# Optimization experiments

Measured on AMD Instinct MI355X. Metric: run time of the kernel, lower is better.

## Reference

```python
import jax, jax.numpy as jnp
import numpy as np

H = 512   # embedding_dim (forced by Attention(512,512))
F = 21    # n_features
T = 28    # output_length

def _cell(x, h, c, Wih, Whh, b):
    # PyTorch LSTMCell math, gate order i,f,g,o
    g = x @ Wih.T + h @ Whh.T + b
    i, f, gg, o = jnp.split(g, 4, axis=-1)
    c2 = jax.nn.sigmoid(f) * c + jax.nn.sigmoid(i) * jnp.tanh(gg)
    h2 = jax.nn.sigmoid(o) * jnp.tanh(c2)
    return h2, c2

def _lstm3(inp, h, c, Wih0, Wih1, Wih2, Whh, bih, bhh):
    # 3-layer LSTM, single time step. h,c: [3,1,H]
    Wihs = (Wih0, Wih1, Wih2)
    hs, cs = [], []
    x = inp
    for l in range(3):
        hl, cl = _cell(x, h[l], c[l], Wihs[l], Whh[l], bih[l] + bhh[l])
        hs.append(hl); cs.append(cl)
        x = hl
    return x, jnp.stack(hs), jnp.stack(cs)

def setup_inputs() -> dict:
    key = jax.random.key(0)
    ks = jax.random.split(key, 20)
    s = 0.05
    f32 = jnp.float32
    return {
        "x": jax.random.normal(ks[0], (1, F), f32),
        "prev_y": jax.random.normal(ks[1], (1, F), f32),
        "enc_Wih0": jax.random.normal(ks[2], (4*H, F), f32) * s,
        "enc_Wih1": jax.random.normal(ks[3], (4*H, H), f32) * s,
        "enc_Wih2": jax.random.normal(ks[4], (4*H, H), f32) * s,
        "enc_Whh": jax.random.normal(ks[5], (3, 4*H, H), f32) * s,
        "enc_bih": jax.random.normal(ks[6], (3, 4*H), f32) * s,
        "enc_bhh": jax.random.normal(ks[7], (3, 4*H), f32) * s,
        "attn_W": jax.random.normal(ks[8], (H, 2*H), f32) * s,
        "attn_b": jax.random.normal(ks[9], (H,), f32) * s,
        "v_W": jax.random.normal(ks[10], (1, H), f32) * s,
        "dec_Wih0": jax.random.normal(ks[11], (4*H, H+F), f32) * s,
        "dec_Wih1": jax.random.normal(ks[12], (4*H, H), f32) * s,
        "dec_Wih2": jax.random.normal(ks[13], (4*H, H), f32) * s,
        "dec_Whh": jax.random.normal(ks[14], (3, 4*H, H), f32) * s,
        "dec_bih": jax.random.normal(ks[15], (3, 4*H), f32) * s,
        "dec_bhh": jax.random.normal(ks[16], (3, 4*H), f32) * s,
        "out_W": jax.random.normal(ks[17], (F, 2*H), f32) * s,
        "out_b": jax.random.normal(ks[18], (F,), f32) * s,
    }

def reference(x, prev_y, enc_Wih0, enc_Wih1, enc_Wih2, enc_Whh, enc_bih, enc_bhh,
              attn_W, attn_b, v_W, dec_Wih0, dec_Wih1, dec_Wih2, dec_Whh, dec_bih, dec_bhh,
              out_W, out_b):
    z = jnp.zeros((3, 1, H), x.dtype)
    # Encoder: single time step over feature-as-sequence input [1, F]
    enc_out, h, c = _lstm3(x, z, z, enc_Wih0, enc_Wih1, enc_Wih2, enc_Whh, enc_bih, enc_bhh)
    # enc_out: [1, H]; src_len == 1

    def step(carry, _):
        prev_out, h, c = carry
        # Bahdanau attention (src_len = 1)
        cat = jnp.concatenate([h[2], enc_out], axis=-1)          # [1, 2H]
        energy = jnp.tanh(cat @ attn_W.T + attn_b)               # [1, H]
        score = energy @ v_W.T                                    # [1, 1]
        a = jax.nn.softmax(score, axis=1)                         # [1, 1] (== 1)
        weighted = a * enc_out                                    # [1, H]
        rnn_in = jnp.concatenate([prev_out, weighted], axis=-1)  # [1, H+F]
        out, h2, c2 = _lstm3(rnn_in, h, c, dec_Wih0, dec_Wih1, dec_Wih2, dec_Whh, dec_bih, dec_bhh)
        y = jnp.concatenate([out, weighted], axis=-1) @ out_W.T + out_b  # [1, F]
        return (y, h2, c2), y

    _, ys = jax.lax.scan(step, (prev_y, h, c), None, length=T)
    return ys  # [T, 1, F]
```

## Files before the change

kernel.cpp:

```cpp
#include <hip/hip_runtime.h>
#include <cstddef>

constexpr int H  = 512;
constexpr int F  = 21;
constexpr int T  = 28;
constexpr int PB = 128;
constexpr int NB = PB + 1;
constexpr int NT = 256;
constexpr int NW = NT / 64;

#define SCOPE_AGENT __HIP_MEMORY_SCOPE_AGENT

__device__ unsigned long long g_hp[2][3][H];
__device__ unsigned long long g_hy[T][H];
__device__ unsigned g_exit;

struct P {
  const float *x, *py, *eW0, *eW1, *eW2, *ebih, *ebhh;
  const float *dW0, *dW1, *dW2, *dWhh, *dbih, *dbhh, *outW, *outb;
  float* out;
};

__device__ __forceinline__ float sigm(float v)  { return 1.0f / (1.0f + __expf(-v)); }
__device__ __forceinline__ float tanh_f(float v){ return 1.0f - 2.0f / (__expf(2.0f * v) + 1.0f); }

__device__ __forceinline__ float4 wredsum4(float4 v) {
#pragma unroll
  for (int off = 32; off > 0; off >>= 1) {
    v.x += __shfl_xor(v.x, off, 64);
    v.y += __shfl_xor(v.y, off, 64);
    v.z += __shfl_xor(v.z, off, 64);
    v.w += __shfl_xor(v.w, off, 64);
  }
  return v;
}
__device__ __forceinline__ float wredsum1(float v) {
#pragma unroll
  for (int off = 32; off > 0; off >>= 1) v += __shfl_xor(v, off, 64);
  return v;
}

__device__ __forceinline__ void pput(unsigned long long* slot, float v, unsigned tag) {
  union { float f; unsigned u; } c; c.f = v;
  unsigned long long pk = ((unsigned long long)tag << 32) | (unsigned long long)c.u;
  (void)__hip_atomic_exchange(slot, pk, __ATOMIC_RELAXED, SCOPE_AGENT);
}
__device__ __forceinline__ unsigned long long tld(const unsigned long long* q) {
  return __hip_atomic_load(q, __ATOMIC_RELAXED, SCOPE_AGENT);
}
__device__ __forceinline__ float fbits(unsigned long long v) {
  union { unsigned u; float f; } c; c.u = (unsigned)v; return c.f;
}

__device__ __forceinline__ void stagev(const unsigned long long* __restrict__ A,
                                       unsigned wa, float* __restrict__ dst) {
  const int i = threadIdx.x;
  unsigned long long v0 = tld(A + i), v1 = tld(A + i + NT);
  int guard = 0;
  while ((((unsigned)(v0 >> 32)) != wa || ((unsigned)(v1 >> 32)) != wa) &&
         ++guard < (1 << 20)) {
    v0 = tld(A + i); v1 = tld(A + i + NT);
  }
  dst[i] = fbits(v0); dst[i + NT] = fbits(v1);
  __syncthreads();
}

struct W8 { float4 a[4]; float4 b[4]; };

__device__ __forceinline__ W8 ldw_g(const float* __restrict__ W, int r, int lane) {
  W8 o;
#pragma unroll
  for (int g = 0; g < 4; ++g) {
    const float* q = W + (size_t)(g * H + r) * H + lane * 8;
    o.a[g] = *(const float4*)q;
    o.b[g] = *(const float4*)(q + 4);
  }
  return o;
}
__device__ __forceinline__ W8 ldw_lds(const float* sM, int w, int lane) {
  W8 o;
#pragma unroll
  for (int g = 0; g < 4; ++g) {
    const float* q = sM + (w * 4 + g) * H + lane * 8;
    o.a[g] = *(const float4*)q;
    o.b[g] = *(const float4*)(q + 4);
  }
  return o;
}
__device__ __forceinline__ void fma8(const W8& wt, const float4& x0, const float4& x1,
                                     float s[4]) {
#pragma unroll
  for (int g = 0; g < 4; ++g) {
    s[g] += wt.a[g].x * x0.x + wt.a[g].y * x0.y + wt.a[g].z * x0.z + wt.a[g].w * x0.w
          + wt.b[g].x * x1.x + wt.b[g].y * x1.y + wt.b[g].z * x1.z + wt.b[g].w * x1.w;
  }
}

__device__ __forceinline__ float cellup(const float4& v, const float b[4], float& c) {
  float cn = sigm(v.y + b[1]) * c + sigm(v.x + b[0]) * tanh_f(v.z + b[2]);
  c = cn;
  return sigm(v.w + b[3]) * tanh_f(cn);
}

__device__ __forceinline__ void write_y_frag(const P& p, int trow, int w, int lane,
                                             const float4& h0, const float4& h1,
                                             const float* sYe) {
  for (int j = w; j < F; j += NW) {
    const float* q = p.outW + (size_t)j * (2 * H) + lane * 8;
    float4 w0 = *(const float4*)q;
    float4 w1 = *(const float4*)(q + 4);
    float s = w0.x * h0.x + w0.y * h0.y + w0.z * h0.z + w0.w * h0.w
            + w1.x * h1.x + w1.y * h1.y + w1.z * h1.z + w1.w * h1.w;
    s = wredsum1(s);
    if (lane == 0) p.out[trow * F + j] = s + sYe[j];
  }
}

__global__ __launch_bounds__(NT, 1)
void k_flow(P p) {
  const int lane = threadIdx.x & 63;
  const int w    = threadIdx.x >> 6;

  __shared__ float sM[NW * 4 * H];
  __shared__ float sBuf[2][H];
  __shared__ float senc[H];
  __shared__ float sYe[F + 3];
  __shared__ int   s_last;

  if (blockIdx.x == PB) {
    stagev(g_hp[1][2], 1u, senc);
    {
      float4 e0 = *(const float4*)(senc + lane * 8);
      float4 e1 = *(const float4*)(senc + lane * 8 + 4);
      for (int j = w; j < F; j += NW) {
        const float* q = p.outW + (size_t)j * (2 * H) + H + lane * 8;
        float4 w0 = *(const float4*)q;
        float4 w1 = *(const float4*)(q + 4);
        float s = w0.x * e0.x + w0.y * e0.y + w0.z * e0.z + w0.w * e0.w
                + w1.x * e1.x + w1.y * e1.y + w1.z * e1.z + w1.w * e1.w;
        s = wredsum1(s);
        if (lane == 0) sYe[j] = s + p.outb[j];
      }
      __syncthreads();
    }
    for (int t = 0; t < T; ++t) {
      float* xb = sBuf[t & 1];
      stagev(g_hy[t], (unsigned)(t + 2), xb);
      float4 h20 = *(const float4*)(xb + lane * 8);
      float4 h21 = *(const float4*)(xb + lane * 8 + 4);
      write_y_frag(p, t, w, lane, h20, h21, sYe);
    }
  } else {
    const int r = blockIdx.x * NW + w;

    float c0 = 0.f, c1 = 0.f, c2 = 0.f;
    float b00[4], b0p[4], b1s[4], b2s[4];
    float sOld0[4] = {0, 0, 0, 0}, sOld1[4] = {0, 0, 0, 0}, sOld2[4] = {0, 0, 0, 0};
    int bi = 0;

    {
      float s0 = 0.f, s1 = 0.f, s2 = 0.f, s3 = 0.f;
      if (lane < F) {
        const float xv = p.x[lane];
        s0 = p.eW0[(size_t)(0 * H + r) * F + lane] * xv;
        s1 = p.eW0[(size_t)(1 * H + r) * F + lane] * xv;
        s2 = p.eW0[(size_t)(2 * H + r) * F + lane] * xv;
        s3 = p.eW0[(size_t)(3 * H + r) * F + lane] * xv;
      }
      float4 v = wredsum4(make_float4(s0, s1, s2, s3));
      if (lane == 0) {
        const float* bi_ = p.ebih + r;
        const float* bh_ = p.ebhh + r;
        float cn = sigm(v.x + bi_[0] + bh_[0]) * tanh_f(v.z + bi_[2 * H] + bh_[2 * H]);
        c0 = cn;
        pput(&g_hp[1][0][r], sigm(v.w + bi_[3 * H] + bh_[3 * H]) * tanh_f(cn), 1u);
      }
    }

    {
      float4 mA[4], mB[4];
#pragma unroll
      for (int g = 0; g < 4; ++g) {
        mA[g] = make_float4(0.f, 0.f, 0.f, 0.f);
        mB[g] = make_float4(0.f, 0.f, 0.f, 0.f);
      }
      for (int f = 0; f < F; ++f) {
        const float* q = p.outW + (size_t)f * (2 * H) + lane * 8;
        const float4 oa = *(const float4*)q;
        const float4 ob = *(const float4*)(q + 4);
#pragma unroll
        for (int g = 0; g < 4; ++g) {
          const float wf = p.dW0[(size_t)(g * H + r) * (H + F) + f];
          mA[g].x += wf * oa.x; mA[g].y += wf * oa.y; mA[g].z += wf * oa.z; mA[g].w += wf * oa.w;
          mB[g].x += wf * ob.x; mB[g].y += wf * ob.y; mB[g].z += wf * ob.z; mB[g].w += wf * ob.w;
        }
      }
#pragma unroll
      for (int g = 0; g < 4; ++g) {
        *(float4*)(sM + (w * 4 + g) * H + lane * 8)     = mA[g];
        *(float4*)(sM + (w * 4 + g) * H + lane * 8 + 4) = mB[g];
      }
    }
#pragma unroll
    for (int g = 0; g < 4; ++g) {
      b1s[g] = p.dbih[4 * H + g * H + r] + p.dbhh[4 * H + g * H + r];
      b2s[g] = p.dbih[8 * H + g * H + r] + p.dbhh[8 * H + g * H + r];
    }

    {
      W8 wt = ldw_g(p.eW1, r, lane);
      stagev(g_hp[1][0], 1u, sBuf[0]);
      float4 a0 = *(const float4*)(sBuf[0] + lane * 8);
      float4 a1 = *(const float4*)(sBuf[0] + lane * 8 + 4);
      float s[4] = {0.f, 0.f, 0.f, 0.f};
      fma8(wt, a0, a1, s);
      float4 v = wredsum4(make_float4(s[0], s[1], s[2], s[3]));
      if (lane == 0) {
        const float* bi_ = p.ebih + 4 * H + r;
        const float* bh_ = p.ebhh + 4 * H + r;
        float cn = sigm(v.x + bi_[0] + bh_[0]) * tanh_f(v.z + bi_[2 * H] + bh_[2 * H]);
        c1 = cn;
        pput(&g_hp[1][1][r], sigm(v.w + bi_[3 * H] + bh_[3 * H]) * tanh_f(cn), 1u);
      }
    }

    {
      W8 wt  = ldw_g(p.eW2, r, lane);
      W8 wh1 = ldw_g(p.dWhh + (size_t)4 * H * H, r, lane);
      stagev(g_hp[1][1], 1u, sBuf[1]);
      float4 a0 = *(const float4*)(sBuf[1] + lane * 8);
      float4 a1 = *(const float4*)(sBuf[1] + lane * 8 + 4);
      float s[4] = {0.f, 0.f, 0.f, 0.f};
      fma8(wt, a0, a1, s);
      float4 v = wredsum4(make_float4(s[0], s[1], s[2], s[3]));
      if (lane == 0) {
        const float* bi_ = p.ebih + 8 * H + r;
        const float* bh_ = p.ebhh + 8 * H + r;
        float cn = sigm(v.x + bi_[0] + bh_[0]) * tanh_f(v.z + bi_[2 * H] + bh_[2 * H]);
        c2 = cn;
        pput(&g_hp[1][2][r], sigm(v.w + bi_[3 * H] + bh_[3 * H]) * tanh_f(cn), 1u);
      }
      fma8(wh1, a0, a1, sOld1);
    }

    {
      W8 wh2 = ldw_g(p.dWhh + (size_t)8 * H * H, r, lane);
      stagev(g_hp[1][2], 1u, senc);
      float4 e0 = *(const float4*)(senc + lane * 8);
      float4 e1 = *(const float4*)(senc + lane * 8 + 4);
      for (int j = w; j < F; j += NW) {
        const float* q = p.outW + (size_t)j * (2 * H) + H + lane * 8;
        float4 w0 = *(const float4*)q;
        float4 w1 = *(const float4*)(q + 4);
        float s = w0.x * e0.x + w0.y * e0.y + w0.z * e0.z + w0.w * e0.w
                + w1.x * e1.x + w1.y * e1.y + w1.z * e1.z + w1.w * e1.w;
        s = wredsum1(s);
        if (lane == 0) sYe[j] = s + p.outb[j];
      }
      {
        float sg[4];
#pragma unroll
        for (int g = 0; g < 4; ++g) {
          const float* q = p.dW0 + (size_t)(g * H + r) * (H + F) + F + lane * 8;
          sg[g] = q[0] * e0.x + q[1] * e0.y + q[2] * e0.z + q[3] * e0.w
                + q[4] * e1.x + q[5] * e1.y + q[6] * e1.z + q[7] * e1.w;
        }
        float4 v = wredsum4(make_float4(sg[0], sg[1], sg[2], sg[3]));
        if (lane == 0) {
          b0p[0] = v.x + p.dbih[0 * H + r] + p.dbhh[0 * H + r];
          b0p[1] = v.y + p.dbih[1 * H + r] + p.dbhh[1 * H + r];
          b0p[2] = v.z + p.dbih[2 * H + r] + p.dbhh[2 * H + r];
          b0p[3] = v.w + p.dbih[3 * H + r] + p.dbhh[3 * H + r];
        }
      }
      {
        float f0 = 0.f, f1 = 0.f, f2 = 0.f, f3 = 0.f;
        if (lane < F) {
          const float yv = p.py[lane];
          f0 = p.dW0[(size_t)(0 * H + r) * (H + F) + lane] * yv;
          f1 = p.dW0[(size_t)(1 * H + r) * (H + F) + lane] * yv;
          f2 = p.dW0[(size_t)(2 * H + r) * (H + F) + lane] * yv;
          f3 = p.dW0[(size_t)(3 * H + r) * (H + F) + lane] * yv;
        }
        float4 v = wredsum4(make_float4(f0, f1, f2, f3));
        if (lane == 0) {
          b00[0] = b0p[0] + v.x; b00[1] = b0p[1] + v.y;
          b00[2] = b0p[2] + v.z; b00[3] = b0p[3] + v.w;
        }
      }
      __syncthreads();
      {
        float f0 = 0.f, f1 = 0.f, f2 = 0.f, f3 = 0.f;
        if (lane < F) {
          const float yv = sYe[lane];
          f0 = p.dW0[(size_t)(0 * H + r) * (H + F) + lane] * yv;
          f1 = p.dW0[(size_t)(1 * H + r) * (H + F) + lane] * yv;
          f2 = p.dW0[(size_t)(2 * H + r) * (H + F) + lane] * yv;
          f3 = p.dW0[(size_t)(3 * H + r) * (H + F) + lane] * yv;
        }
        float4 v = wredsum4(make_float4(f0, f1, f2, f3));
        if (lane == 0) {
          b0p[0] += v.x; b0p[1] += v.y; b0p[2] += v.z; b0p[3] += v.w;
        }
      }
      fma8(wh2, e0, e1, sOld2);
    }

    {
      W8 wh0 = ldw_g(p.dWhh, r, lane);
      float4 a0 = *(const float4*)(sBuf[0] + lane * 8);
      float4 a1 = *(const float4*)(sBuf[0] + lane * 8 + 4);
      float s[4] = {0.f, 0.f, 0.f, 0.f};
      fma8(wh0, a0, a1, s);
      float4 v = wredsum4(make_float4(s[0], s[1], s[2], s[3]));
      if (lane == 0) pput(&g_hp[0][0][r], cellup(v, b00, c0), 2u);
    }
    __syncthreads();

    for (int t = 0; t < T; ++t) {
      const int pb = t & 1, ob = pb ^ 1;
      const unsigned wn = (unsigned)(t + 2);
      const unsigned wo = (unsigned)(t + 1);

      if (t >= 1) {
        W8 wh2 = ldw_g(p.dWhh + (size_t)8 * H * H, r, lane);
        stagev(g_hp[ob][2], wo, sBuf[bi]);
        W8 wm = ldw_lds(sM, w, lane);
        float4 h20 = *(const float4*)(sBuf[bi] + lane * 8);
        float4 h21 = *(const float4*)(sBuf[bi] + lane * 8 + 4);
        float s[4] = {sOld0[0], sOld0[1], sOld0[2], sOld0[3]};
        fma8(wm, h20, h21, s);
        float4 v = wredsum4(make_float4(s[0], s[1], s[2], s[3]));
        if (lane == 0) pput(&g_hp[pb][0][r], cellup(v, b0p, c0), wn);
        sOld2[0] = sOld2[1] = sOld2[2] = sOld2[3] = 0.f;
        fma8(wh2, h20, h21, sOld2);
        bi ^= 1;
      }

      {
        W8 wi  = ldw_g(p.dW1, r, lane);
        W8 wh0 = ldw_g(p.dWhh, r, lane);
        stagev(g_hp[pb][0], wn, sBuf[bi]);
        float4 a0 = *(const float4*)(sBuf[bi] + lane * 8);
        float4 a1 = *(const float4*)(sBuf[bi] + lane * 8 + 4);
        float s[4] = {sOld1[0], sOld1[1], sOld1[2], sOld1[3]};
        fma8(wi, a0, a1, s);
        float4 v = wredsum4(make_float4(s[0], s[1], s[2], s[3]));
        if (lane == 0) pput(&g_hp[pb][1][r], cellup(v, b1s, c1), wn);
        sOld0[0] = sOld0[1] = sOld0[2] = sOld0[3] = 0.f;
        fma8(wh0, a0, a1, sOld0);
        bi ^= 1;
      }
      {
        W8 wi  = ldw_g(p.dW2, r, lane);
        W8 wh1 = ldw_g(p.dWhh + (size_t)4 * H * H, r, lane);
        stagev(g_hp[pb][1], wn, sBuf[bi]);
        float4 a0 = *(const float4*)(sBuf[bi] + lane * 8);
        float4 a1 = *(const float4*)(sBuf[bi] + lane * 8 + 4);
        float s[4] = {sOld2[0], sOld2[1], sOld2[2], sOld2[3]};
        fma8(wi, a0, a1, s);
        float4 v = wredsum4(make_float4(s[0], s[1], s[2], s[3]));
        if (lane == 0) {
          float hv = cellup(v, b2s, c2);
          pput(&g_hp[pb][2][r], hv, wn);
          pput(&g_hy[t][r], hv, wn);
        }
        sOld1[0] = sOld1[1] = sOld1[2] = sOld1[3] = 0.f;
        fma8(wh1, a0, a1, sOld1);
        bi ^= 1;
      }
    }
  }

  __syncthreads();
  if (threadIdx.x == 0) {
    unsigned old = __hip_atomic_fetch_add(&g_exit, 1u, __ATOMIC_RELAXED, SCOPE_AGENT);
    s_last = (old == NB - 1) ? 1 : 0;
  }
  __syncthreads();
  if (s_last) {
    unsigned long long* z = &g_hp[0][0][0];
    for (int i = threadIdx.x; i < 2 * 3 * H; i += NT)
      __hip_atomic_store(z + i, 0ull, __ATOMIC_RELAXED, SCOPE_AGENT);
    unsigned long long* y = &g_hy[0][0];
    for (int i = threadIdx.x; i < T * H; i += NT)
      __hip_atomic_store(y + i, 0ull, __ATOMIC_RELAXED, SCOPE_AGENT);
    if (threadIdx.x == 0)
      __hip_atomic_store(&g_exit, 0u, __ATOMIC_RELAXED, SCOPE_AGENT);
  }
}

extern "C" void kernel_launch(void* const* d_in, const int* in_sizes, int n_in,
                              void* d_out, int out_size, void* d_ws, size_t ws_size,
                              hipStream_t stream) {
  P p;
  p.x    = (const float*)d_in[0];
  p.py   = (const float*)d_in[1];
  p.eW0  = (const float*)d_in[2];
  p.eW1  = (const float*)d_in[3];
  p.eW2  = (const float*)d_in[4];
  p.ebih = (const float*)d_in[6];
  p.ebhh = (const float*)d_in[7];
  p.dW0  = (const float*)d_in[11];
  p.dW1  = (const float*)d_in[12];
  p.dW2  = (const float*)d_in[13];
  p.dWhh = (const float*)d_in[14];
  p.dbih = (const float*)d_in[15];
  p.dbhh = (const float*)d_in[16];
  p.outW = (const float*)d_in[17];
  p.outb = (const float*)d_in[18];
  p.out  = (float*)d_out;

  hipLaunchKernelGGL(k_flow, dim3(NB), dim3(NT), 0, stream, p);
}
```

Measured before the change: 319.6 us.

## Epoch-tag flags, vectorize polling loads, keep weights in registers, drop exit cleanup

The per-launch zeroing of the flag arrays at kernel exit is replaced by an epoch counter folded into the tags, which removes the end-of-kernel atomic count and reset pass. Flag polling now uses a single 16-byte load with the sc1 cache bit per thread instead of two 8-byte atomic loads. The fused output-to-input matrix and the W1/W2 tiles stay in registers across all steps instead of being reread from LDS and global memory. Stage waits are moved ahead of the remaining weight loads. This raises register pressure and relies on the epoch never wrapping into stale tags.

```diff
diff --git a/kernel.cpp b/kernel.cpp
--- a/kernel.cpp
+++ b/kernel.cpp
@@ -11,9 +11,9 @@
 
 #define SCOPE_AGENT __HIP_MEMORY_SCOPE_AGENT
 
-__device__ unsigned long long g_hp[2][3][H];
-__device__ unsigned long long g_hy[T][H];
-__device__ unsigned g_exit;
+__device__ __align__(16) unsigned long long g_hp[2][3][H];
+__device__ __align__(16) unsigned long long g_hy[T][H];
+__device__ unsigned g_epoch;
 
 struct P {
   const float *x, *py, *eW0, *eW1, *eW2, *ebih, *ebhh;
@@ -45,23 +45,23 @@
   unsigned long long pk = ((unsigned long long)tag << 32) | (unsigned long long)c.u;
   (void)__hip_atomic_exchange(slot, pk, __ATOMIC_RELAXED, SCOPE_AGENT);
 }
-__device__ __forceinline__ unsigned long long tld(const unsigned long long* q) {
-  return __hip_atomic_load(q, __ATOMIC_RELAXED, SCOPE_AGENT);
-}
-__device__ __forceinline__ float fbits(unsigned long long v) {
-  union { unsigned u; float f; } c; c.u = (unsigned)v; return c.f;
+
+typedef unsigned int u32x4 __attribute__((ext_vector_type(4)));
+__device__ __forceinline__ u32x4 tld16(const unsigned long long* q) {
+  u32x4 r;
+  asm volatile("global_load_dwordx4 %0, %1, off sc1\n\t"
+               "s_waitcnt vmcnt(0)"
+               : "=v"(r) : "v"(q) : "memory");
+  return r;
 }
 
 __device__ __forceinline__ void stagev(const unsigned long long* __restrict__ A,
                                        unsigned wa, float* __restrict__ dst) {
   const int i = threadIdx.x;
-  unsigned long long v0 = tld(A + i), v1 = tld(A + i + NT);
+  u32x4 v = tld16(A + 2 * i);
   int guard = 0;
-  while ((((unsigned)(v0 >> 32)) != wa || ((unsigned)(v1 >> 32)) != wa) &&
-         ++guard < (1 << 20)) {
-    v0 = tld(A + i); v1 = tld(A + i + NT);
-  }
-  dst[i] = fbits(v0); dst[i + NT] = fbits(v1);
+  while ((v.y != wa || v.w != wa) && ++guard < (1 << 20)) v = tld16(A + 2 * i);
+  *(float2*)(dst + 2 * i) = make_float2(__uint_as_float(v.x), __uint_as_float(v.z));
   __syncthreads();
 }
 
@@ -72,16 +72,6 @@
 #pragma unroll
   for (int g = 0; g < 4; ++g) {
     const float* q = W + (size_t)(g * H + r) * H + lane * 8;
-    o.a[g] = *(const float4*)q;
-    o.b[g] = *(const float4*)(q + 4);
-  }
-  return o;
-}
-__device__ __forceinline__ W8 ldw_lds(const float* sM, int w, int lane) {
-  W8 o;
-#pragma unroll
-  for (int g = 0; g < 4; ++g) {
-    const float* q = sM + (w * 4 + g) * H + lane * 8;
     o.a[g] = *(const float4*)q;
     o.b[g] = *(const float4*)(q + 4);
   }
@@ -120,15 +110,15 @@
 void k_flow(P p) {
   const int lane = threadIdx.x & 63;
   const int w    = threadIdx.x >> 6;
-
-  __shared__ float sM[NW * 4 * H];
+  const unsigned ep =
+      __hip_atomic_load(&g_epoch, __ATOMIC_RELAXED, SCOPE_AGENT) << 6;
+
   __shared__ float sBuf[2][H];
   __shared__ float senc[H];
   __shared__ float sYe[F + 3];
-  __shared__ int   s_last;
 
   if (blockIdx.x == PB) {
-    stagev(g_hp[1][2], 1u, senc);
+    stagev(g_hp[1][2], ep + 1u, senc);
     {
       float4 e0 = *(const float4*)(senc + lane * 8);
       float4 e1 = *(const float4*)(senc + lane * 8 + 4);
@@ -145,11 +135,13 @@
     }
     for (int t = 0; t < T; ++t) {
       float* xb = sBuf[t & 1];
-      stagev(g_hy[t], (unsigned)(t + 2), xb);
+      stagev(g_hy[t], ep + (unsigned)(t + 2), xb);
       float4 h20 = *(const float4*)(xb + lane * 8);
       float4 h21 = *(const float4*)(xb + lane * 8 + 4);
       write_y_frag(p, t, w, lane, h20, h21, sYe);
     }
+    if (threadIdx.x == 0)
+      __hip_atomic_fetch_add(&g_epoch, 1u, __ATOMIC_RELAXED, SCOPE_AGENT);
   } else {
     const int r = blockIdx.x * NW + w;
 
@@ -173,34 +165,34 @@
         const float* bh_ = p.ebhh + r;
         float cn = sigm(v.x + bi_[0] + bh_[0]) * tanh_f(v.z + bi_[2 * H] + bh_[2 * H]);
         c0 = cn;
-        pput(&g_hp[1][0][r], sigm(v.w + bi_[3 * H] + bh_[3 * H]) * tanh_f(cn), 1u);
-      }
-    }
-
-    {
-      float4 mA[4], mB[4];
+        pput(&g_hp[1][0][r], sigm(v.w + bi_[3 * H] + bh_[3 * H]) * tanh_f(cn), ep + 1u);
+      }
+    }
+
+    W8 wM;
+    {
 #pragma unroll
       for (int g = 0; g < 4; ++g) {
-        mA[g] = make_float4(0.f, 0.f, 0.f, 0.f);
-        mB[g] = make_float4(0.f, 0.f, 0.f, 0.f);
+        wM.a[g] = make_float4(0.f, 0.f, 0.f, 0.f);
+        wM.b[g] = make_float4(0.f, 0.f, 0.f, 0.f);
       }
       for (int f = 0; f < F; ++f) {
         const float* q = p.outW + (size_t)f * (2 * H) + lane * 8;
-        const float4 oa = *(const float4*)q;
-        const float4 ob = *(const float4*)(q + 4);
+        const float4 oa  = *(const float4*)q;
+        const float4 obv = *(const float4*)(q + 4);
 #pragma unroll
         for (int g = 0; g < 4; ++g) {
           const float wf = p.dW0[(size_t)(g * H + r) * (H + F) + f];
-          mA[g].x += wf * oa.x; mA[g].y += wf * oa.y; mA[g].z += wf * oa.z; mA[g].w += wf * oa.w;
-          mB[g].x += wf * ob.x; mB[g].y += wf * ob.y; mB[g].z += wf * ob.z; mB[g].w += wf * ob.w;
-        }
-      }
-#pragma unroll
-      for (int g = 0; g < 4; ++g) {
-        *(float4*)(sM + (w * 4 + g) * H + lane * 8)     = mA[g];
-        *(float4*)(sM + (w * 4 + g) * H + lane * 8 + 4) = mB[g];
-      }
-    }
+          wM.a[g].x += wf * oa.x;  wM.a[g].y += wf * oa.y;
+          wM.a[g].z += wf * oa.z;  wM.a[g].w += wf * oa.w;
+          wM.b[g].x += wf * obv.x; wM.b[g].y += wf * obv.y;
+          wM.b[g].z += wf * obv.z; wM.b[g].w += wf * obv.w;
+        }
+      }
+    }
+    W8 wD1 = ldw_g(p.dW1, r, lane);
+    W8 wD2 = ldw_g(p.dW2, r, lane);
+
 #pragma unroll
     for (int g = 0; g < 4; ++g) {
       b1s[g] = p.dbih[4 * H + g * H + r] + p.dbhh[4 * H + g * H + r];
@@ -209,7 +201,7 @@
 
     {
       W8 wt = ldw_g(p.eW1, r, lane);
-      stagev(g_hp[1][0], 1u, sBuf[0]);
+      stagev(g_hp[1][0], ep + 1u, sBuf[0]);
       float4 a0 = *(const float4*)(sBuf[0] + lane * 8);
       float4 a1 = *(const float4*)(sBuf[0] + lane * 8 + 4);
       float s[4] = {0.f, 0.f, 0.f, 0.f};
@@ -220,14 +212,14 @@
         const float* bh_ = p.ebhh + 4 * H + r;
         float cn = sigm(v.x + bi_[0] + bh_[0]) * tanh_f(v.z + bi_[2 * H] + bh_[2 * H]);
         c1 = cn;
-        pput(&g_hp[1][1][r], sigm(v.w + bi_[3 * H] + bh_[3 * H]) * tanh_f(cn), 1u);
+        pput(&g_hp[1][1][r], sigm(v.w + bi_[3 * H] + bh_[3 * H]) * tanh_f(cn), ep + 1u);
       }
     }
 
     {
       W8 wt  = ldw_g(p.eW2, r, lane);
       W8 wh1 = ldw_g(p.dWhh + (size_t)4 * H * H, r, lane);
-      stagev(g_hp[1][1], 1u, sBuf[1]);
+      stagev(g_hp[1][1], ep + 1u, sBuf[1]);
       float4 a0 = *(const float4*)(sBuf[1] + lane * 8);
       float4 a1 = *(const float4*)(sBuf[1] + lane * 8 + 4);
       float s[4] = {0.f, 0.f, 0.f, 0.f};
@@ -238,14 +230,15 @@
         const float* bh_ = p.ebhh + 8 * H + r;
         float cn = sigm(v.x + bi_[0] + bh_[0]) * tanh_f(v.z + bi_[2 * H] + bh_[2 * H]);
         c2 = cn;
-        pput(&g_hp[1][2][r], sigm(v.w + bi_[3 * H] + bh_[3 * H]) * tanh_f(cn), 1u);
+        pput(&g_hp[1][2][r], sigm(v.w + bi_[3 * H] + bh_[3 * H]) * tanh_f(cn), ep + 1u);
       }
       fma8(wh1, a0, a1, sOld1);
     }
 
+    W8 wh00;
     {
       W8 wh2 = ldw_g(p.dWhh + (size_t)8 * H * H, r, lane);
-      stagev(g_hp[1][2], 1u, senc);
+      stagev(g_hp[1][2], ep + 1u, senc);
       float4 e0 = *(const float4*)(senc + lane * 8);
       float4 e1 = *(const float4*)(senc + lane * 8 + 4);
       for (int j = w; j < F; j += NW) {
@@ -273,6 +266,7 @@
           b0p[3] = v.w + p.dbih[3 * H + r] + p.dbhh[3 * H + r];
         }
       }
+      wh00 = ldw_g(p.dWhh, r, lane);
       {
         float f0 = 0.f, f1 = 0.f, f2 = 0.f, f3 = 0.f;
         if (lane < F) {
@@ -307,29 +301,27 @@
     }
 
     {
-      W8 wh0 = ldw_g(p.dWhh, r, lane);
       float4 a0 = *(const float4*)(sBuf[0] + lane * 8);
       float4 a1 = *(const float4*)(sBuf[0] + lane * 8 + 4);
       float s[4] = {0.f, 0.f, 0.f, 0.f};
-      fma8(wh0, a0, a1, s);
+      fma8(wh00, a0, a1, s);
       float4 v = wredsum4(make_float4(s[0], s[1], s[2], s[3]));
-      if (lane == 0) pput(&g_hp[0][0][r], cellup(v, b00, c0), 2u);
+      if (lane == 0) pput(&g_hp[0][0][r], cellup(v, b00, c0), ep + 2u);
     }
     __syncthreads();
 
     for (int t = 0; t < T; ++t) {
       const int pb = t & 1, ob = pb ^ 1;
-      const unsigned wn = (unsigned)(t + 2);
-      const unsigned wo = (unsigned)(t + 1);
+      const unsigned wn = ep + (unsigned)(t + 2);
+      const unsigned wo = wn - 1u;
 
       if (t >= 1) {
+        stagev(g_hp[ob][2], wo, sBuf[bi]);
         W8 wh2 = ldw_g(p.dWhh + (size_t)8 * H * H, r, lane);
-        stagev(g_hp[ob][2], wo, sBuf[bi]);
-        W8 wm = ldw_lds(sM, w, lane);
         float4 h20 = *(const float4*)(sBuf[bi] + lane * 8);
         float4 h21 = *(const float4*)(sBuf[bi] + lane * 8 + 4);
         float s[4] = {sOld0[0], sOld0[1], sOld0[2], sOld0[3]};
-        fma8(wm, h20, h21, s);
+        fma8(wM, h20, h21, s);
         float4 v = wredsum4(make_float4(s[0], s[1], s[2], s[3]));
         if (lane == 0) pput(&g_hp[pb][0][r], cellup(v, b0p, c0), wn);
         sOld2[0] = sOld2[1] = sOld2[2] = sOld2[3] = 0.f;
@@ -338,13 +330,12 @@
       }
 
       {
-        W8 wi  = ldw_g(p.dW1, r, lane);
+        stagev(g_hp[pb][0], wn, sBuf[bi]);
         W8 wh0 = ldw_g(p.dWhh, r, lane);
-        stagev(g_hp[pb][0], wn, sBuf[bi]);
         float4 a0 = *(const float4*)(sBuf[bi] + lane * 8);
         float4 a1 = *(const float4*)(sBuf[bi] + lane * 8 + 4);
         float s[4] = {sOld1[0], sOld1[1], sOld1[2], sOld1[3]};
-        fma8(wi, a0, a1, s);
+        fma8(wD1, a0, a1, s);
         float4 v = wredsum4(make_float4(s[0], s[1], s[2], s[3]));
         if (lane == 0) pput(&g_hp[pb][1][r], cellup(v, b1s, c1), wn);
         sOld0[0] = sOld0[1] = sOld0[2] = sOld0[3] = 0.f;
@@ -352,13 +343,12 @@
         bi ^= 1;
       }
       {
-        W8 wi  = ldw_g(p.dW2, r, lane);
+        stagev(g_hp[pb][1], wn, sBuf[bi]);
         W8 wh1 = ldw_g(p.dWhh + (size_t)4 * H * H, r, lane);
-        stagev(g_hp[pb][1], wn, sBuf[bi]);
         float4 a0 = *(const float4*)(sBuf[bi] + lane * 8);
         float4 a1 = *(const float4*)(sBuf[bi] + lane * 8 + 4);
         float s[4] = {sOld2[0], sOld2[1], sOld2[2], sOld2[3]};
-        fma8(wi, a0, a1, s);
+        fma8(wD2, a0, a1, s);
         float4 v = wredsum4(make_float4(s[0], s[1], s[2], s[3]));
         if (lane == 0) {
           float hv = cellup(v, b2s, c2);
@@ -370,23 +360,6 @@
         bi ^= 1;
       }
     }
-  }
-
-  __syncthreads();
-  if (threadIdx.x == 0) {
-    unsigned old = __hip_atomic_fetch_add(&g_exit, 1u, __ATOMIC_RELAXED, SCOPE_AGENT);
-    s_last = (old == NB - 1) ? 1 : 0;
-  }
-  __syncthreads();
-  if (s_last) {
-    unsigned long long* z = &g_hp[0][0][0];
-    for (int i = threadIdx.x; i < 2 * 3 * H; i += NT)
-      __hip_atomic_store(z + i, 0ull, __ATOMIC_RELAXED, SCOPE_AGENT);
-    unsigned long long* y = &g_hy[0][0];
-    for (int i = threadIdx.x; i < T * H; i += NT)
-      __hip_atomic_store(y + i, 0ull, __ATOMIC_RELAXED, SCOPE_AGENT);
-    if (threadIdx.x == 0)
-      __hip_atomic_store(&g_exit, 0u, __ATOMIC_RELAXED, SCOPE_AGENT);
   }
 }
 
```

Result: slower. 333.8 us (+4.4%).
